# Kernel tuning notes

Hardware: AMD Instinct MI355X
Metric: run time of the kernel (lower is better)

The kernel has to match this reference:

```python
import jax, jax.numpy as jnp
import numpy as np
import math

B, L, IN, HID, NLAYERS, AA = 16, 512, 512, 512, 6, 21
KAPPA_ADD = 5.0


def _sru_layer(x, W, v, b):
    # x: [L, B, din]; W: [din, 2*HID*k]; v, b: [2(gate f/r), 2(dir), HID]
    Lx, Bx, din = x.shape
    d = HID
    k = W.shape[1] // (2 * d)  # 4 if projecting residual, 3 if residual = input
    U = (x @ W).reshape(Lx, Bx, 2, d, k)
    res = U[..., 3] if k == 4 else x.reshape(Lx, Bx, 2, d)
    # time-flip direction 1 so a single scan handles both directions
    flip = lambda a: jnp.concatenate([a[:, :, :1], a[::-1, :, 1:]], axis=2)
    u0, u1, u2, resf = flip(U[..., 0]), flip(U[..., 1]), flip(U[..., 2]), flip(res)
    vf, vr = v[0], v[1]
    bf, br = b[0], b[1]

    def step(c, t):
        u0t, u1t, u2t, rt = t
        f = jax.nn.sigmoid(u1t + vf * c + bf)
        c1 = f * c + (1.0 - f) * u0t
        r = jax.nn.sigmoid(u2t + vr * c1 + br)
        h = r * c1 + (1.0 - r) * rt
        return c1, h

    c0 = jnp.zeros((Bx, 2, d), x.dtype)
    _, H = jax.lax.scan(step, c0, (u0, u1, u2, resf))
    return flip(H).reshape(Lx, Bx, 2 * d)


def setup_inputs():
    key = jax.random.key(0)
    inp = {}
    inp['input'] = jax.random.normal(jax.random.fold_in(key, 0), (B, L, IN), jnp.float32)
    inp['hidden'] = jnp.zeros((NLAYERS, B, 2 * HID), jnp.float32)
    for l in range(NLAYERS):
        din = IN if l == 0 else 2 * HID
        k = 4 if din != 2 * HID else 3
        inp[f'sru_w{l}'] = jax.random.normal(jax.random.fold_in(key, 10 + l), (din, 2 * HID * k), jnp.float32) * (1.0 / math.sqrt(din))
        inp[f'sru_v{l}'] = jax.random.normal(jax.random.fold_in(key, 20 + l), (2, 2, HID), jnp.float32) * 0.1
        inp[f'sru_b{l}'] = jnp.zeros((2, 2, HID), jnp.float32)

    def lin(seed, din, dout):
        w = jax.random.normal(jax.random.fold_in(key, seed), (din, dout), jnp.float32) * (1.0 / math.sqrt(din))
        return w, jnp.zeros((dout,), jnp.float32)

    inp['fc1_logits_w'], inp['fc1_logits_b'] = lin(30, 2 * HID, HID)
    inp['fc2_logits_w'], inp['fc2_logits_b'] = lin(31, HID, AA)
    inp['fc1_angles_w'], inp['fc1_angles_b'] = lin(32, 2 * HID, HID)
    inp['fc2_means_w'], inp['fc2_means_b'] = lin(33, HID, 2)
    inp['fc2_kappas_w'], inp['fc2_kappas_b'] = lin(34, HID, 2)
    return inp


def reference(input, hidden, sru_w0, sru_v0, sru_b0, sru_w1, sru_v1, sru_b1, sru_w2, sru_v2, sru_b2, sru_w3, sru_v3, sru_b3, sru_w4, sru_v4, sru_b4, sru_w5, sru_v5, sru_b5, fc1_logits_w, fc1_logits_b, fc2_logits_w, fc2_logits_b, fc1_angles_w, fc1_angles_b, fc2_means_w, fc2_means_b, fc2_kappas_w, fc2_kappas_b):
    x = input.transpose(1, 0, 2)  # [L, B, IN]
    ws = [sru_w0, sru_w1, sru_w2, sru_w3, sru_w4, sru_w5]
    vs = [sru_v0, sru_v1, sru_v2, sru_v3, sru_v4, sru_v5]
    bs = [sru_b0, sru_b1, sru_b2, sru_b3, sru_b4, sru_b5]
    for W, v, b in zip(ws, vs, bs):
        x = _sru_layer(x, W, v, b)
    sru_out = x.transpose(1, 0, 2)  # [B, L, 2*HID]
    h_log = sru_out @ fc1_logits_w + fc1_logits_b
    output_logits = jax.nn.log_softmax(h_log @ fc2_logits_w + fc2_logits_b, axis=-1)
    h_ang = sru_out @ fc1_angles_w + fc1_angles_b
    output_means = jnp.tanh(h_ang @ fc2_means_w + fc2_means_b) * math.pi
    output_kappas = KAPPA_ADD + jax.nn.softplus(h_ang @ fc2_kappas_w + fc2_kappas_b)
    return (output_logits, output_means, output_kappas)
```

## Files before the change

### kernel.cpp

```cpp
#include <hip/hip_runtime.h>

typedef __attribute__((ext_vector_type(8))) short short8;
typedef __attribute__((ext_vector_type(4))) float f32x4;

__device__ __forceinline__ ushort f2bf(float x) {
  unsigned u = __builtin_bit_cast(unsigned, x);
  u = (u + 0x7fffu + ((u >> 16) & 1u)) >> 16;
  return (ushort)u;
}
__device__ __forceinline__ float bf2f(ushort x) {
  return __builtin_bit_cast(float, ((unsigned)x) << 16);
}

#define AS1CP(p) ((const __attribute__((address_space(1))) unsigned int*)(p))
#define AS3CP(p) ((__attribute__((address_space(3))) unsigned int*)(p))
#define GLDS(g, l, SZ) __builtin_amdgcn_global_load_lds(AS1CP(g), AS3CP(l), SZ, 0, 0)

__global__ __launch_bounds__(256) void k_cvt(const float* __restrict__ in,
                                             ushort* __restrict__ out, int n4) {
  int i = blockIdx.x * 256 + threadIdx.x;
  if (i >= n4) return;
  float4 v = reinterpret_cast<const float4*>(in)[i];
  ushort4 o;
  o.x = f2bf(v.x); o.y = f2bf(v.y); o.z = f2bf(v.z); o.w = f2bf(v.w);
  reinterpret_cast<ushort4*>(out)[i] = o;
}

__global__ __launch_bounds__(256) void k_transpose(const float* __restrict__ W,
                                                   ushort* __restrict__ Wt,
                                                   int N, int K) {
  __shared__ float tile[32][33];
  int bx = blockIdx.x * 32;
  int by = blockIdx.y * 32;
  int tx = threadIdx.x, ty = threadIdx.y;
#pragma unroll
  for (int i = 0; i < 32; i += 8)
    tile[ty + i][tx] = W[(size_t)(by + ty + i) * N + bx + tx];
  __syncthreads();
#pragma unroll
  for (int i = 0; i < 32; i += 8)
    Wt[(size_t)(bx + ty + i) * K + by + tx] = f2bf(tile[tx][ty + i]);
}

template <int KKp>
__global__ __launch_bounds__(256) void k_transpose_sru(const float* __restrict__ W,
                                                       ushort* __restrict__ Wt,
                                                       int N, int K) {
  __shared__ float tile[32][33];
  int bx = blockIdx.x * 32;
  int by = blockIdx.y * 32;
  int tx = threadIdx.x, ty = threadIdx.y;
#pragma unroll
  for (int i = 0; i < 32; i += 8)
    tile[ty + i][tx] = W[(size_t)(by + ty + i) * N + bx + tx];
  __syncthreads();
#pragma unroll
  for (int i = 0; i < 32; i += 8) {
    int c = bx + ty + i;
    int ch = c / KKp, j = c - ch * KKp;
    int nc = (j < 2) ? (ch * 2 + j) : ((j == 2) ? (2048 + ch) : (3072 + ch));
    Wt[(size_t)nc * K + by + tx] = f2bf(tile[tx][ty + i]);
  }
}

template <int BF16OUT>
__global__ __launch_bounds__(256) void k_gemm(const ushort* __restrict__ A,
                                              const ushort* __restrict__ Bt,
                                              void* __restrict__ Cv,
                                              int K, int N) {
  __shared__ __align__(16) ushort lsA[2][2][4096];
  __shared__ __align__(16) ushort lsB[2][2][4096];
  const int tid = threadIdx.x;
  const int bm = blockIdx.x, bn = blockIdx.y;
  const int w = tid >> 6, l = tid & 63;
  const int wm = (w >> 1) * 64, wn = (w & 1) * 64;
  const int lr = l & 15, lg = l >> 4;
  f32x4 acc[4][4] = {};
  const int srow = tid >> 2;
  const int scol = (((tid & 3) ^ ((srow >> 1) & 3))) * 8;
  const ushort* Ag = A + (size_t)(bm * 128 + srow) * K + scol;
  const ushort* Bg = Bt + (size_t)(bn * 128 + srow) * K + scol;
  const int nt = K >> 6;
  const int rxor = (lr >> 1) & 3;

#define GEMM_ISSUE(SL, KT)                                                  \
  {                                                                         \
    GLDS(Ag + (KT), &lsA[SL][0][w * 512], 16);                              \
    GLDS(Ag + (size_t)64 * K + (KT), &lsA[SL][0][2048 + w * 512], 16);      \
    GLDS(Bg + (KT), &lsB[SL][0][w * 512], 16);                              \
    GLDS(Bg + (size_t)64 * K + (KT), &lsB[SL][0][2048 + w * 512], 16);      \
    GLDS(Ag + (KT) + 32, &lsA[SL][1][w * 512], 16);                         \
    GLDS(Ag + (size_t)64 * K + (KT) + 32, &lsA[SL][1][2048 + w * 512], 16); \
    GLDS(Bg + (KT) + 32, &lsB[SL][1][w * 512], 16);                         \
    GLDS(Bg + (size_t)64 * K + (KT) + 32, &lsB[SL][1][2048 + w * 512], 16); \
  }

  GEMM_ISSUE(0, 0);
  for (int t = 0; t < nt; ++t) {
    const int cur = t & 1;
    if (t + 1 < nt) {
      GEMM_ISSUE(cur ^ 1, (t + 1) * 64);
      asm volatile("s_waitcnt vmcnt(8)" ::: "memory");
    } else {
      asm volatile("s_waitcnt vmcnt(0)" ::: "memory");
    }
    asm volatile("s_barrier" ::: "memory");
#pragma unroll
    for (int kk = 0; kk < 2; ++kk) {
      short8 af[4], bfr[4];
#pragma unroll
      for (int i = 0; i < 4; ++i)
        af[i] = *(const short8*)&lsA[cur][kk][(wm + i * 16 + lr) * 32 + ((lg ^ rxor) * 8)];
#pragma unroll
      for (int j = 0; j < 4; ++j)
        bfr[j] = *(const short8*)&lsB[cur][kk][(wn + j * 16 + lr) * 32 + ((lg ^ rxor) * 8)];
#pragma unroll
      for (int i = 0; i < 4; ++i)
#pragma unroll
        for (int j = 0; j < 4; ++j)
          acc[i][j] = __builtin_amdgcn_mfma_f32_16x16x32_bf16(af[i], bfr[j], acc[i][j], 0, 0, 0);
    }
    asm volatile("s_barrier" ::: "memory");
  }
#undef GEMM_ISSUE
  const size_t cbase = (size_t)(bm * 128 + wm + lg * 4) * N + bn * 128 + wn + lr;
  if (BF16OUT) {
    ushort* Cb = (ushort*)Cv + cbase;
#pragma unroll
    for (int i = 0; i < 4; ++i)
#pragma unroll
      for (int j = 0; j < 4; ++j)
#pragma unroll
        for (int r = 0; r < 4; ++r)
          Cb[(size_t)(i * 16 + r) * N + j * 16] = f2bf(acc[i][j][r]);
  } else {
    float* Cb = (float*)Cv + cbase;
#pragma unroll
    for (int i = 0; i < 4; ++i)
#pragma unroll
      for (int j = 0; j < 4; ++j)
#pragma unroll
        for (int r = 0; r < 4; ++r)
          Cb[(size_t)(i * 16 + r) * N + j * 16] = acc[i][j][r];
  }
}

__global__ __launch_bounds__(64, 1) void sru_rec8(const ushort* __restrict__ U, int NU,
                                                  const ushort* __restrict__ R, int RS,
                                                  const float* __restrict__ v,
                                                  const float* __restrict__ bb,
                                                  ushort* __restrict__ H) {
  const int lane = threadIdx.x;
  const int blk = blockIdx.x;
  const int b = blk >> 4, rem = blk & 15, dir = rem >> 3, cg = rem & 7;
  const int ch = dir * 512 + cg * 64 + lane;
  const float vf = v[ch], vr = v[1024 + ch];
  const float bfv = bb[ch], brv = bb[1024 + ch];
  const float vfn = -vf, vrn = -vr;
  const float kf0 = -bfv, kr0 = -brv;
  const int tstep = dir ? -1 : 1;
  const int t0 = dir ? 511 : 0;
  const ushort* U01 = U + (size_t)b * 512 * NU + ch * 2;
  const ushort* U2  = U + (size_t)b * 512 * NU + 2048 + ch;
  const ushort* Rb  = R + (size_t)b * 512 * RS + ch;
  ushort* Hb = H + (size_t)b * 512 * 1024 + ch;

  unsigned q01[4][8];
  ushort q2[4][8], qr[4][8];

#define SR_ISSUE(J, TI)                                                        \
  {                                                                            \
    const int base_ = (TI) * 8;                                                \
    _Pragma("unroll")                                                          \
    for (int t = 0; t < 8; ++t) {                                              \
      int tt = t0 + tstep * (base_ + t);                                       \
      q01[J][t] = *(const unsigned*)(U01 + (size_t)tt * NU);                   \
      q2[J][t] = U2[(size_t)tt * NU];                                          \
      qr[J][t] = Rb[(size_t)tt * RS];                                          \
    }                                                                          \
  }

#define SR_COMP(J, TI)                                                         \
  {                                                                            \
    _Pragma("unroll")                                                          \
    for (int s = 0; s < 8; ++s) {                                              \
      float u0 = __builtin_bit_cast(float, q01[J][s] << 16);                   \
      float u1 = __builtin_bit_cast(float, q01[J][s] & 0xffff0000u);           \
      float u2 = bf2f(q2[J][s]);                                               \
      float uR = bf2f(qr[J][s]);                                               \
      float ef = __expf(__builtin_fmaf(vfn, c, kf0 - u1));                     \
      float f = __builtin_amdgcn_rcpf(1.f + ef);                               \
      c = __builtin_fmaf(f, c - u0, u0);                                       \
      float er = __expf(__builtin_fmaf(vrn, c, kr0 - u2));                     \
      float r = __builtin_amdgcn_rcpf(1.f + er);                               \
      float hh = __builtin_fmaf(r, c - uR, uR);                                \
      Hb[(size_t)(t0 + tstep * ((TI) * 8 + s)) * 1024] = f2bf(hh);             \
    }                                                                          \
  }

  SR_ISSUE(0, 0)
  SR_ISSUE(1, 1)
  SR_ISSUE(2, 2)
  float c = 0.f;
#pragma unroll 1
  for (int ii = 0; ii < 15; ++ii) {
#define TILE_J(J)                                                              \
    {                                                                          \
      const int i = ii * 4 + (J);                                              \
      SR_ISSUE((((J) + 3) & 3), i + 3)                                         \
      asm volatile("s_waitcnt vmcnt(63)" ::: "memory");                        \
      SR_COMP(J, i)                                                            \
    }
    TILE_J(0) TILE_J(1) TILE_J(2) TILE_J(3)
#undef TILE_J
  }
  SR_ISSUE(3, 63)
  asm volatile("s_waitcnt vmcnt(63)" ::: "memory");
  SR_COMP(0, 60)
  asm volatile("s_waitcnt vmcnt(48)" ::: "memory");
  SR_COMP(1, 61)
  asm volatile("s_waitcnt vmcnt(24)" ::: "memory");
  SR_COMP(2, 62)
  asm volatile("s_waitcnt vmcnt(0)" ::: "memory");
  SR_COMP(3, 63)
#undef SR_ISSUE
#undef SR_COMP
}

__global__ __launch_bounds__(256) void k_buildW2(const float* __restrict__ w2l,
                                                 const float* __restrict__ w2m,
                                                 const float* __restrict__ w2k,
                                                 ushort* __restrict__ Wt2) {
  int i = blockIdx.x * 256 + threadIdx.x;
  if (i >= 128 * 1024) return;
  int n = i >> 10, k = i & 1023;
  float vv = 0.f;
  if (n < 21 && k < 512) vv = w2l[k * 21 + n];
  else if (n >= 21 && n < 23 && k >= 512) vv = w2m[(k - 512) * 2 + (n - 21)];
  else if (n >= 23 && n < 25 && k >= 512) vv = w2k[(k - 512) * 2 + (n - 23)];
  Wt2[i] = f2bf(vv);
}

__global__ __launch_bounds__(64) void k_bias25(const float* __restrict__ b1l,
                                               const float* __restrict__ b1a,
                                               const float* __restrict__ w2l,
                                               const float* __restrict__ b2l,
                                               const float* __restrict__ w2m,
                                               const float* __restrict__ b2m,
                                               const float* __restrict__ w2k,
                                               const float* __restrict__ b2k,
                                               float* __restrict__ b2adj) {
  int o = threadIdx.x;
  if (o >= 25) return;
  float s;
  if (o < 21) {
    s = b2l[o];
    for (int k = 0; k < 512; ++k) s += b1l[k] * w2l[k * 21 + o];
  } else if (o < 23) {
    s = b2m[o - 21];
    for (int k = 0; k < 512; ++k) s += b1a[k] * w2m[k * 2 + (o - 21)];
  } else {
    s = b2k[o - 23];
    for (int k = 0; k < 512; ++k) s += b1a[k] * w2k[k * 2 + (o - 23)];
  }
  b2adj[o] = s;
}

__global__ __launch_bounds__(64) void k_act(const float* __restrict__ T,
                                            const float* __restrict__ b2adj,
                                            float* __restrict__ out) {
  const int row = blockIdx.x;
  const int lane = threadIdx.x;
  float myv = 0.f;
  if (lane < 25) myv = T[(size_t)row * 128 + lane] + b2adj[lane];
  float x = (lane < 21) ? myv : -1e30f;
#pragma unroll
  for (int off = 32; off; off >>= 1) x = fmaxf(x, __shfl_xor(x, off));
  float e = (lane < 21) ? expf(myv - x) : 0.f;
#pragma unroll
  for (int off = 32; off; off >>= 1) e += __shfl_xor(e, off);
  float lse = x + logf(e);
  if (lane < 21) {
    out[(size_t)row * 21 + lane] = myv - lse;
  } else if (lane < 23) {
    out[172032 + row * 2 + (lane - 21)] = tanhf(myv) * 3.14159265358979323846f;
  } else if (lane < 25) {
    float sp = (myv > 20.f) ? myv : log1pf(expf(myv));
    out[188416 + row * 2 + (lane - 23)] = 5.f + sp;
  }
}

extern "C" void kernel_launch(void* const* d_in, const int* in_sizes, int n_in,
                              void* d_out, int out_size, void* d_ws, size_t ws_size,
                              hipStream_t stream) {
  (void)in_sizes; (void)n_in; (void)out_size; (void)ws_size;
  const float* input = (const float*)d_in[0];
  const float* sw[6]; const float* sv[6]; const float* sb[6];
  for (int l = 0; l < 6; ++l) {
    sw[l] = (const float*)d_in[2 + 3 * l];
    sv[l] = (const float*)d_in[3 + 3 * l];
    sb[l] = (const float*)d_in[4 + 3 * l];
  }
  const float* fc1lw = (const float*)d_in[20];
  const float* fc1lb = (const float*)d_in[21];
  const float* fc2lw = (const float*)d_in[22];
  const float* fc2lb = (const float*)d_in[23];
  const float* fc1aw = (const float*)d_in[24];
  const float* fc1ab = (const float*)d_in[25];
  const float* fc2mw = (const float*)d_in[26];
  const float* fc2mb = (const float*)d_in[27];
  const float* fc2kw = (const float*)d_in[28];
  const float* fc2kb = (const float*)d_in[29];

  char* ws = (char*)d_ws;
  ushort* U = (ushort*)ws;
  ushort* Hcat2 = (ushort*)ws;
  float* T = (float*)(ws + 67108864);
  ushort* H0 = (ushort*)(ws + 134217728);
  ushort* H1 = (ushort*)(ws + 150994944);
  ushort* X0 = (ushort*)(ws + 167772160);
  const size_t wbase = 176160768;
  ushort* Wtl[6];
  Wtl[0] = (ushort*)(ws + wbase);
  for (int l = 1; l < 6; ++l)
    Wtl[l] = (ushort*)(ws + wbase + 4194304 + (size_t)(l - 1) * 6291456);
  ushort* Wfc = (ushort*)(ws + wbase + 4194304 + 5ull * 6291456);
  ushort* Wt2 = (ushort*)(ws + wbase + 37748736);
  float* b2adj = (float*)(ws + wbase + 38010880);

  k_cvt<<<4096, 256, 0, stream>>>(input, X0, 8192 * 512 / 4);
  k_buildW2<<<512, 256, 0, stream>>>(fc2lw, fc2mw, fc2kw, Wt2);
  k_bias25<<<1, 64, 0, stream>>>(fc1lb, fc1ab, fc2lw, fc2lb, fc2mw, fc2mb,
                                 fc2kw, fc2kb, b2adj);

  k_transpose_sru<4><<<dim3(128, 16), dim3(32, 8), 0, stream>>>(sw[0], Wtl[0], 4096, 512);
  for (int l = 1; l < 6; ++l)
    k_transpose_sru<3><<<dim3(96, 32), dim3(32, 8), 0, stream>>>(sw[l], Wtl[l], 3072, 1024);
  k_transpose<<<dim3(16, 32), dim3(32, 8), 0, stream>>>(fc1lw, Wfc, 512, 1024);
  k_transpose<<<dim3(16, 32), dim3(32, 8), 0, stream>>>(fc1aw, Wfc + (size_t)512 * 1024, 512, 1024);

  for (int l = 0; l < 6; ++l) {
    const ushort* Ain = (l == 0) ? X0 : ((l & 1) ? H0 : H1);
    ushort* Hout = (l & 1) ? H1 : H0;
    int K = (l == 0) ? 512 : 1024;
    int N = (l == 0) ? 4096 : 3072;
    k_gemm<1><<<dim3(64, N / 128), 256, 0, stream>>>(Ain, Wtl[l], U, K, N);
    if (l == 0)
      sru_rec8<<<256, 64, 0, stream>>>(U, 4096, U + 3072, 4096, sv[l], sb[l], Hout);
    else
      sru_rec8<<<256, 64, 0, stream>>>(U, 3072, Ain, 1024, sv[l], sb[l], Hout);
  }

  k_gemm<1><<<dim3(64, 8), 256, 0, stream>>>(H1, Wfc, Hcat2, 1024, 1024);

  k_gemm<0><<<dim3(64, 1), 256, 0, stream>>>(Hcat2, Wt2, T, 1024, 128);

  k_act<<<8192, 64, 0, stream>>>(T, b2adj, (float*)d_out);
}
```

Baseline: 762.2 us.

## Transpose SRU projection output so recurrence reads contiguous time vectors

The projection GEMM now computes U transposed (features by time), with A and B operands swapped, so each channel's time series is contiguous. The recurrence kernel loads 8 timesteps per 16-byte vector load instead of strided scalar loads, and keeps a deeper prefetch pipeline. It also writes a transposed copy of H for the next layer's residual input. The intent is to cut the latency-bound strided memory traffic in the sequential scan, at the cost of an extra H write per layer and a changed GEMM output layout.

```diff
diff --git a/kernel.cpp b/kernel.cpp
--- a/kernel.cpp
+++ b/kernel.cpp
@@ -58,7 +58,7 @@
   for (int i = 0; i < 32; i += 8) {
     int c = bx + ty + i;
     int ch = c / KKp, j = c - ch * KKp;
-    int nc = (j < 2) ? (ch * 2 + j) : ((j == 2) ? (2048 + ch) : (3072 + ch));
+    int nc = j * 1024 + ch;
     Wt[(size_t)nc * K + by + tx] = f2bf(tile[tx][ty + i]);
   }
 }
@@ -145,84 +145,92 @@
   }
 }
 
-__global__ __launch_bounds__(64, 1) void sru_rec8(const ushort* __restrict__ U, int NU,
-                                                  const ushort* __restrict__ R, int RS,
-                                                  const float* __restrict__ v,
-                                                  const float* __restrict__ bb,
-                                                  ushort* __restrict__ H) {
+template <int WRITE_NEXT>
+__global__ __launch_bounds__(64, 1) void sru_rec10(const ushort* __restrict__ U,
+                                                   const ushort* __restrict__ Rp,
+                                                   const float* __restrict__ v,
+                                                   const float* __restrict__ bb,
+                                                   ushort* __restrict__ H,
+                                                   ushort* __restrict__ Hres) {
+  const size_t PL = (size_t)1024 * 8192;
   const int lane = threadIdx.x;
   const int blk = blockIdx.x;
-  const int b = blk >> 4, rem = blk & 15, dir = rem >> 3, cg = rem & 7;
-  const int ch = dir * 512 + cg * 64 + lane;
+  const int b = blk >> 4, cg = blk & 15;
+  const int ch = cg * 64 + lane;
+  const int dir = ch >> 9;
   const float vf = v[ch], vr = v[1024 + ch];
   const float bfv = bb[ch], brv = bb[1024 + ch];
   const float vfn = -vf, vrn = -vr;
   const float kf0 = -bfv, kr0 = -brv;
-  const int tstep = dir ? -1 : 1;
-  const int t0 = dir ? 511 : 0;
-  const ushort* U01 = U + (size_t)b * 512 * NU + ch * 2;
-  const ushort* U2  = U + (size_t)b * 512 * NU + 2048 + ch;
-  const ushort* Rb  = R + (size_t)b * 512 * RS + ch;
+  const size_t rowoff = (size_t)ch * 8192 + b * 512;
+  const ushort* U0 = U + rowoff;
+  const ushort* U1 = U0 + PL;
+  const ushort* U2 = U0 + 2 * PL;
+  const ushort* Rb = Rp + rowoff;
   ushort* Hb = H + (size_t)b * 512 * 1024 + ch;
-
-  unsigned q01[4][8];
-  ushort q2[4][8], qr[4][8];
+  ushort* Hr = Hres + rowoff;
+
+  short8 q0[8], q1[8], q2[8], qr[8];
 
 #define SR_ISSUE(J, TI)                                                        \
   {                                                                            \
-    const int base_ = (TI) * 8;                                                \
-    _Pragma("unroll")                                                          \
-    for (int t = 0; t < 8; ++t) {                                              \
-      int tt = t0 + tstep * (base_ + t);                                       \
-      q01[J][t] = *(const unsigned*)(U01 + (size_t)tt * NU);                   \
-      q2[J][t] = U2[(size_t)tt * NU];                                          \
-      qr[J][t] = Rb[(size_t)tt * RS];                                          \
-    }                                                                          \
+    const int tb_ = dir ? (504 - (TI) * 8) : ((TI) * 8);                       \
+    q0[J] = *(const short8*)(U0 + tb_);                                        \
+    q1[J] = *(const short8*)(U1 + tb_);                                        \
+    q2[J] = *(const short8*)(U2 + tb_);                                        \
+    qr[J] = *(const short8*)(Rb + tb_);                                        \
   }
 
 #define SR_COMP(J, TI)                                                         \
   {                                                                            \
+    const int tb_ = dir ? (504 - (TI) * 8) : ((TI) * 8);                       \
+    short8 hv = {};                                                            \
     _Pragma("unroll")                                                          \
     for (int s = 0; s < 8; ++s) {                                              \
-      float u0 = __builtin_bit_cast(float, q01[J][s] << 16);                   \
-      float u1 = __builtin_bit_cast(float, q01[J][s] & 0xffff0000u);           \
-      float u2 = bf2f(q2[J][s]);                                               \
-      float uR = bf2f(qr[J][s]);                                               \
+      const int e0 = s, e1 = 7 - s;                                            \
+      const int e = dir ? e1 : e0;                                             \
+      float u0 = bf2f((ushort)(dir ? q0[J][e1] : q0[J][e0]));                  \
+      float u1 = bf2f((ushort)(dir ? q1[J][e1] : q1[J][e0]));                  \
+      float u2 = bf2f((ushort)(dir ? q2[J][e1] : q2[J][e0]));                  \
+      float uR = bf2f((ushort)(dir ? qr[J][e1] : qr[J][e0]));                  \
       float ef = __expf(__builtin_fmaf(vfn, c, kf0 - u1));                     \
       float f = __builtin_amdgcn_rcpf(1.f + ef);                               \
       c = __builtin_fmaf(f, c - u0, u0);                                       \
       float er = __expf(__builtin_fmaf(vrn, c, kr0 - u2));                     \
       float r = __builtin_amdgcn_rcpf(1.f + er);                               \
       float hh = __builtin_fmaf(r, c - uR, uR);                                \
-      Hb[(size_t)(t0 + tstep * ((TI) * 8 + s)) * 1024] = f2bf(hh);             \
+      ushort hb = f2bf(hh);                                                    \
+      Hb[(size_t)(tb_ + e) * 1024] = hb;                                       \
+      if (WRITE_NEXT) { if (dir) hv[e1] = (short)hb; else hv[e0] = (short)hb; }\
     }                                                                          \
-  }
-
-  SR_ISSUE(0, 0)
-  SR_ISSUE(1, 1)
-  SR_ISSUE(2, 2)
+    if (WRITE_NEXT) *(short8*)(Hr + tb_) = hv;                                 \
+  }
+
+  SR_ISSUE(0, 0) SR_ISSUE(1, 1) SR_ISSUE(2, 2) SR_ISSUE(3, 3)
+  SR_ISSUE(4, 4) SR_ISSUE(5, 5) SR_ISSUE(6, 6)
   float c = 0.f;
 #pragma unroll 1
-  for (int ii = 0; ii < 15; ++ii) {
+  for (int ii = 0; ii < 7; ++ii) {
 #define TILE_J(J)                                                              \
     {                                                                          \
-      const int i = ii * 4 + (J);                                              \
-      SR_ISSUE((((J) + 3) & 3), i + 3)                                         \
-      asm volatile("s_waitcnt vmcnt(63)" ::: "memory");                        \
+      const int i = ii * 8 + (J);                                              \
+      SR_ISSUE((((J) + 7) & 7), i + 7)                                         \
+      asm volatile("s_waitcnt vmcnt(28)" ::: "memory");                        \
       SR_COMP(J, i)                                                            \
     }
     TILE_J(0) TILE_J(1) TILE_J(2) TILE_J(3)
+    TILE_J(4) TILE_J(5) TILE_J(6) TILE_J(7)
 #undef TILE_J
   }
-  SR_ISSUE(3, 63)
-  asm volatile("s_waitcnt vmcnt(63)" ::: "memory");
-  SR_COMP(0, 60)
-  asm volatile("s_waitcnt vmcnt(48)" ::: "memory");
-  SR_COMP(1, 61)
-  asm volatile("s_waitcnt vmcnt(24)" ::: "memory");
-  SR_COMP(2, 62)
-  asm volatile("s_waitcnt vmcnt(0)" ::: "memory");
-  SR_COMP(3, 63)
+  SR_ISSUE(7, 63)
+  asm volatile("s_waitcnt vmcnt(28)" ::: "memory"); SR_COMP(0, 56)
+  asm volatile("s_waitcnt vmcnt(24)" ::: "memory"); SR_COMP(1, 57)
+  asm volatile("s_waitcnt vmcnt(20)" ::: "memory"); SR_COMP(2, 58)
+  asm volatile("s_waitcnt vmcnt(16)" ::: "memory"); SR_COMP(3, 59)
+  asm volatile("s_waitcnt vmcnt(12)" ::: "memory"); SR_COMP(4, 60)
+  asm volatile("s_waitcnt vmcnt(8)" ::: "memory");  SR_COMP(5, 61)
+  asm volatile("s_waitcnt vmcnt(4)" ::: "memory");  SR_COMP(6, 62)
+  asm volatile("s_waitcnt vmcnt(0)" ::: "memory");  SR_COMP(7, 63)
 #undef SR_ISSUE
 #undef SR_COMP
 }
@@ -315,7 +323,9 @@
   char* ws = (char*)d_ws;
   ushort* U = (ushort*)ws;
   ushort* Hcat2 = (ushort*)ws;
-  float* T = (float*)(ws + 67108864);
+  float* T = (float*)(ws + 33554432);
+  ushort* HresA = (ushort*)(ws + 67108864);
+  ushort* HresB = (ushort*)(ws + 83886080);
   ushort* H0 = (ushort*)(ws + 134217728);
   ushort* H1 = (ushort*)(ws + 150994944);
   ushort* X0 = (ushort*)(ws + 167772160);
@@ -339,16 +349,19 @@
   k_transpose<<<dim3(16, 32), dim3(32, 8), 0, stream>>>(fc1lw, Wfc, 512, 1024);
   k_transpose<<<dim3(16, 32), dim3(32, 8), 0, stream>>>(fc1aw, Wfc + (size_t)512 * 1024, 512, 1024);
 
+  const size_t PL = (size_t)1024 * 8192;
   for (int l = 0; l < 6; ++l) {
     const ushort* Ain = (l == 0) ? X0 : ((l & 1) ? H0 : H1);
     ushort* Hout = (l & 1) ? H1 : H0;
     int K = (l == 0) ? 512 : 1024;
-    int N = (l == 0) ? 4096 : 3072;
-    k_gemm<1><<<dim3(64, N / 128), 256, 0, stream>>>(Ain, Wtl[l], U, K, N);
-    if (l == 0)
-      sru_rec8<<<256, 64, 0, stream>>>(U, 4096, U + 3072, 4096, sv[l], sb[l], Hout);
+    int NF = (l == 0) ? 4096 : 3072;
+    k_gemm<1><<<dim3(NF / 128, 64), 256, 0, stream>>>(Wtl[l], Ain, U, K, 8192);
+    const ushort* Rp = (l == 0) ? (U + 3 * PL) : ((l & 1) ? HresA : HresB);
+    ushort* Hro = (l & 1) ? HresB : HresA;
+    if (l < 5)
+      sru_rec10<1><<<256, 64, 0, stream>>>(U, Rp, sv[l], sb[l], Hout, Hro);
     else
-      sru_rec8<<<256, 64, 0, stream>>>(U, 3072, Ain, 1024, sv[l], sb[l], Hout);
+      sru_rec10<0><<<256, 64, 0, stream>>>(U, Rp, sv[l], sb[l], Hout, Hro);
   }
 
   k_gemm<1><<<dim3(64, 8), 256, 0, stream>>>(H1, Wfc, Hcat2, 1024, 1024);
```

Result: faster. 743.2 us, median of 3 (-2.5%).
